# Kernel tuning notes

Hardware: AMD Instinct MI355X
Metric: run time of the kernel (lower is better)

The kernel has to match this reference:

```python
import jax, jax.numpy as jnp
import numpy as np

B, M, D, W = 4, 4096, 64, 128  # batch/heads, seq (m=n), head dim (k), nnz per row


def setup_inputs() -> dict:
    key = jax.random.key(0)
    kq, kk, kv, kc = jax.random.split(key, 4)
    q = jax.random.normal(kq, (B, M, D), dtype=jnp.float32)
    k = jax.random.normal(kk, (B, M, D), dtype=jnp.float32)
    v = jax.random.normal(kv, (B, M, D), dtype=jnp.float32)
    # CSR with uniform W nonzeros per row: row_offsets = arange(M+1)*W implicit,
    # column_indices flattened is [M*W]; stored here as [M, W].
    column_indices = jax.random.randint(kc, (M, W), 0, M).astype(jnp.int32)
    return {"q": q, "k": k, "v": v, "column_indices": column_indices}


def reference(q, k, v, column_indices):
    # SDDMM: logits[b,i,w] = <q[b,i,:], k[b, col[i,w], :]> at sparse positions only
    k_g = k[:, column_indices, :]                      # [B, M, W, D]
    logits = jnp.einsum('bmd,bmwd->bmw', q, k_g)       # sparse values per row
    # Sparse row-wise softmax (each CSR row has exactly W entries)
    weights = jax.nn.softmax(logits, axis=-1)          # [B, M, W]
    # SpMM: out[b,i,d] = sum_w weights[b,i,w] * v[b, col[i,w], d]
    v_g = v[:, column_indices, :]                      # [B, M, W, D]
    out = jnp.einsum('bmw,bmwd->bmd', weights, v_g)    # [B, M, D]
    return out
```

## Files before the change

kernel.cpp:

```cpp
#include <hip/hip_runtime.h>
#include <hip/hip_fp16.h>
#include <math.h>

constexpr int B = 4;
constexpr int M = 4096;
constexpr int D = 64;
constexpr int W = 128;
constexpr int NELEM = B * M * D;

__global__ __launch_bounds__(256) void cvt_f32_f16_2(
    const float4* __restrict__ k, const float4* __restrict__ v,
    __half2* __restrict__ kh, __half2* __restrict__ vh, int n4) {
    int i = blockIdx.x * 256 + threadIdx.x;
    const float4* src;
    __half2* dst;
    if (i < n4) { src = k; dst = kh; }
    else        { src = v; dst = vh; i -= n4; if (i >= n4) return; }
    float4 f = src[i];
    dst[2 * i]     = __floats2half2_rn(f.x, f.y);
    dst[2 * i + 1] = __floats2half2_rn(f.z, f.w);
}

__global__ __launch_bounds__(256, 4) void sparse_attn_f16(
    const float* __restrict__ q,
    const __half* __restrict__ kh,
    const __half* __restrict__ vh,
    const int*   __restrict__ idx,
    float*       __restrict__ out)
{
    const int blk  = blockIdx.x;
    const int b    = blk & 3;
    const int mb   = (blk >> 2) * 4;
    const int t    = threadIdx.x;
    const int wave = t >> 6;
    const int lane = t & 63;
    const int ci   = lane & 7;
    const int r    = lane >> 3;
    const int m    = mb + wave;

    __shared__ int idx_s[4 * W];

    ((int2*)idx_s)[t] = ((const int2*)(idx + (size_t)mb * W))[t];

    const float* qrow = q + ((size_t)b * M + m) * D;
    const float4 qa = ((const float4*)qrow)[2 * ci];
    const float4 qb = ((const float4*)qrow)[2 * ci + 1];

    __syncthreads();

    int off[16];
    #pragma unroll
    for (int j = 0; j < 16; ++j) off[j] = idx_s[wave * W + j * 8 + r];

    const __half* kb = kh + (size_t)b * M * D;
    const __half* vb = vh + (size_t)b * M * D;

    float larr[16];
    #pragma unroll
    for (int batch = 0; batch < 2; ++batch) {
        float4 kreg[8];
        #pragma unroll
        for (int jj = 0; jj < 8; ++jj) {
            const int j = batch * 8 + jj;
            kreg[jj] = *(const float4*)(kb + (size_t)off[j] * D + ci * 8);
        }
        #pragma unroll
        for (int jj = 0; jj < 8; ++jj) {
            const __half2* h = (const __half2*)&kreg[jj];
            float2 f0 = __half22float2(h[0]);
            float2 f1 = __half22float2(h[1]);
            float2 f2 = __half22float2(h[2]);
            float2 f3 = __half22float2(h[3]);
            float part = f0.x * qa.x + f0.y * qa.y + f1.x * qa.z + f1.y * qa.w
                       + f2.x * qb.x + f2.y * qb.y + f3.x * qb.z + f3.y * qb.w;
            part += __shfl_xor(part, 1);
            part += __shfl_xor(part, 2);
            part += __shfl_xor(part, 4);
            larr[batch * 8 + jj] = part;
        }
    }

    float mx = larr[0];
    #pragma unroll
    for (int j = 1; j < 16; ++j) mx = fmaxf(mx, larr[j]);
    mx = fmaxf(mx, __shfl_xor(mx, 8));
    mx = fmaxf(mx, __shfl_xor(mx, 16));
    mx = fmaxf(mx, __shfl_xor(mx, 32));

    float sum = 0.f;
    #pragma unroll
    for (int j = 0; j < 16; ++j) { larr[j] = __expf(larr[j] - mx); sum += larr[j]; }
    sum += __shfl_xor(sum, 8);
    sum += __shfl_xor(sum, 16);
    sum += __shfl_xor(sum, 32);
    const float inv = 1.0f / sum;

    float acc[8] = {0, 0, 0, 0, 0, 0, 0, 0};
    #pragma unroll
    for (int batch = 0; batch < 2; ++batch) {
        float4 vreg[8];
        #pragma unroll
        for (int jj = 0; jj < 8; ++jj) {
            const int j = batch * 8 + jj;
            vreg[jj] = *(const float4*)(vb + (size_t)off[j] * D + ci * 8);
        }
        #pragma unroll
        for (int jj = 0; jj < 8; ++jj) {
            const float p = larr[batch * 8 + jj];
            const __half2* h = (const __half2*)&vreg[jj];
            #pragma unroll
            for (int c = 0; c < 4; ++c) {
                float2 f = __half22float2(h[c]);
                acc[2 * c]     += p * f.x;
                acc[2 * c + 1] += p * f.y;
            }
        }
    }
    #pragma unroll
    for (int o = 8; o < 64; o <<= 1) {
        #pragma unroll
        for (int i = 0; i < 8; ++i) acc[i] += __shfl_xor(acc[i], o);
    }

    if (r == 0) {
        float4* orow = (float4*)(out + ((size_t)b * M + m) * D);
        orow[2 * ci]     = make_float4(acc[0] * inv, acc[1] * inv,
                                       acc[2] * inv, acc[3] * inv);
        orow[2 * ci + 1] = make_float4(acc[4] * inv, acc[5] * inv,
                                       acc[6] * inv, acc[7] * inv);
    }
}

__global__ __launch_bounds__(128) void sparse_attn_f32(
    const float* __restrict__ q,
    const float* __restrict__ k,
    const float* __restrict__ v,
    const int*   __restrict__ idx,
    float*       __restrict__ out)
{
    const int blk = blockIdx.x;
    const int b = blk & 3;
    const int m = blk >> 2;
    const int t = threadIdx.x;
    const int lane = t & 63;
    const int wave = t >> 6;
    const int ci = lane & 15;
    const int r  = lane >> 4;

    __shared__ int   idx_s[W];
    __shared__ float sc_s[W];
    __shared__ float red_s[4];
    __shared__ float4 opart_s[16];

    idx_s[t] = idx[m * W + t];
    const float4 qf = ((const float4*)(q + ((size_t)b * M + m) * D))[ci];
    __syncthreads();

    const float* kb = k + (size_t)b * M * D;
    const int wbase = wave * 64;

    #pragma unroll
    for (int j = 0; j < 16; ++j) {
        const int w = wbase + j * 4 + r;
        const float4 kv = ((const float4*)(kb + (size_t)idx_s[w] * D))[ci];
        float part = kv.x * qf.x + kv.y * qf.y + kv.z * qf.z + kv.w * qf.w;
        part += __shfl_xor(part, 1);
        part += __shfl_xor(part, 2);
        part += __shfl_xor(part, 4);
        part += __shfl_xor(part, 8);
        if (ci == 0) sc_s[w] = part;
    }
    __syncthreads();

    float logit = sc_s[t];
    float mx = logit;
    #pragma unroll
    for (int o = 1; o < 64; o <<= 1) mx = fmaxf(mx, __shfl_xor(mx, o));
    if (lane == 0) red_s[wave] = mx;
    __syncthreads();
    mx = fmaxf(red_s[0], red_s[1]);
    float e = __expf(logit - mx);
    float sm = e;
    #pragma unroll
    for (int o = 1; o < 64; o <<= 1) sm += __shfl_xor(sm, o);
    if (lane == 0) red_s[2 + wave] = sm;
    __syncthreads();
    const float inv_denom = 1.0f / (red_s[2] + red_s[3]);
    sc_s[t] = e * inv_denom;
    __syncthreads();

    const float* vb = v + (size_t)b * M * D;
    float4 acc = {0.f, 0.f, 0.f, 0.f};
    #pragma unroll
    for (int j = 0; j < 16; ++j) {
        const int w = wbase + j * 4 + r;
        const float p = sc_s[w];
        const float4 vv = ((const float4*)(vb + (size_t)idx_s[w] * D))[ci];
        acc.x += p * vv.x; acc.y += p * vv.y;
        acc.z += p * vv.z; acc.w += p * vv.w;
    }
    acc.x += __shfl_xor(acc.x, 16); acc.y += __shfl_xor(acc.y, 16);
    acc.z += __shfl_xor(acc.z, 16); acc.w += __shfl_xor(acc.w, 16);
    acc.x += __shfl_xor(acc.x, 32); acc.y += __shfl_xor(acc.y, 32);
    acc.z += __shfl_xor(acc.z, 32); acc.w += __shfl_xor(acc.w, 32);

    if (wave == 0 && r == 0) opart_s[ci] = acc;
    __syncthreads();
    if (wave == 1 && r == 0) {
        const float4 o0 = opart_s[ci];
        float4 res;
        res.x = o0.x + acc.x; res.y = o0.y + acc.y;
        res.z = o0.z + acc.z; res.w = o0.w + acc.w;
        ((float4*)(out + ((size_t)b * M + m) * D))[ci] = res;
    }
}

extern "C" void kernel_launch(void* const* d_in, const int* in_sizes, int n_in,
                              void* d_out, int out_size, void* d_ws, size_t ws_size,
                              hipStream_t stream) {
    const float* q = (const float*)d_in[0];
    const float* k = (const float*)d_in[1];
    const float* v = (const float*)d_in[2];
    const int* idx = (const int*)d_in[3];
    float* out = (float*)d_out;

    const size_t need = (size_t)2 * NELEM * sizeof(__half);
    if (ws_size >= need) {
        __half* kh = (__half*)d_ws;
        __half* vh = kh + NELEM;
        const int n4 = NELEM / 4;
        const int cblk = (2 * n4 + 255) / 256;
        cvt_f32_f16_2<<<cblk, 256, 0, stream>>>((const float4*)k, (const float4*)v,
                                                (__half2*)kh, (__half2*)vh, n4);
        sparse_attn_f16<<<B * M / 4, 256, 0, stream>>>(q, kh, vh, idx, out);
    } else {
        sparse_attn_f32<<<B * M, 128, 0, stream>>>(q, k, v, idx, out);
    }
}
```

Before: 95.99 us.

## Use fdot2 for QK, nontemporal gathers, and prefetch V before softmax

Converts q to fp16 and computes QK partial dot products with packed fdot2 instead of unpacking each half to float. K and V rows are gathered with nontemporal 128-bit loads using precomputed 32-bit byte offsets. The first batch of V rows is issued before the softmax reduction and the second right after it, so gather latency overlaps the softmax math. Rounding q to fp16 reduces dot-product precision, and the extra in-flight V registers may raise register pressure.

```diff
diff --git a/kernel.cpp b/kernel.cpp
--- a/kernel.cpp
+++ b/kernel.cpp
@@ -7,6 +7,9 @@
 constexpr int D = 64;
 constexpr int W = 128;
 constexpr int NELEM = B * M * D;
+
+typedef _Float16 h2_t __attribute__((ext_vector_type(2)));
+typedef int      i4_t __attribute__((ext_vector_type(4)));
 
 __global__ __launch_bounds__(256) void cvt_f32_f16_2(
     const float4* __restrict__ k, const float4* __restrict__ v,
@@ -45,34 +48,39 @@
     const float* qrow = q + ((size_t)b * M + m) * D;
     const float4 qa = ((const float4*)qrow)[2 * ci];
     const float4 qb = ((const float4*)qrow)[2 * ci + 1];
-
-    __syncthreads();
-
-    int off[16];
-    #pragma unroll
-    for (int j = 0; j < 16; ++j) off[j] = idx_s[wave * W + j * 8 + r];
-
-    const __half* kb = kh + (size_t)b * M * D;
-    const __half* vb = vh + (size_t)b * M * D;
+    h2_t qh[4];
+    qh[0] = (h2_t){(_Float16)qa.x, (_Float16)qa.y};
+    qh[1] = (h2_t){(_Float16)qa.z, (_Float16)qa.w};
+    qh[2] = (h2_t){(_Float16)qb.x, (_Float16)qb.y};
+    qh[3] = (h2_t){(_Float16)qb.z, (_Float16)qb.w};
+
+    __syncthreads();
+
+    int voff[16];
+    #pragma unroll
+    for (int j = 0; j < 16; ++j)
+        voff[j] = idx_s[wave * W + j * 8 + r] * (D * 2) + ci * 16;
+
+    const char* kb = (const char*)(kh + (size_t)b * M * D);
+    const char* vb = (const char*)(vh + (size_t)b * M * D);
 
     float larr[16];
     #pragma unroll
     for (int batch = 0; batch < 2; ++batch) {
-        float4 kreg[8];
+        i4_t kreg[8];
+        #pragma unroll
+        for (int jj = 0; jj < 8; ++jj)
+            kreg[jj] = __builtin_nontemporal_load(
+                (const i4_t*)(kb + voff[batch * 8 + jj]));
         #pragma unroll
         for (int jj = 0; jj < 8; ++jj) {
-            const int j = batch * 8 + jj;
-            kreg[jj] = *(const float4*)(kb + (size_t)off[j] * D + ci * 8);
-        }
-        #pragma unroll
-        for (int jj = 0; jj < 8; ++jj) {
-            const __half2* h = (const __half2*)&kreg[jj];
-            float2 f0 = __half22float2(h[0]);
-            float2 f1 = __half22float2(h[1]);
-            float2 f2 = __half22float2(h[2]);
-            float2 f3 = __half22float2(h[3]);
-            float part = f0.x * qa.x + f0.y * qa.y + f1.x * qa.z + f1.y * qa.w
-                       + f2.x * qb.x + f2.y * qb.y + f3.x * qb.z + f3.y * qb.w;
+            union { i4_t v; h2_t h[4]; } u;
+            u.v = kreg[jj];
+            float part = 0.f;
+            part = __builtin_amdgcn_fdot2(u.h[0], qh[0], part, false);
+            part = __builtin_amdgcn_fdot2(u.h[1], qh[1], part, false);
+            part = __builtin_amdgcn_fdot2(u.h[2], qh[2], part, false);
+            part = __builtin_amdgcn_fdot2(u.h[3], qh[3], part, false);
             part += __shfl_xor(part, 1);
             part += __shfl_xor(part, 2);
             part += __shfl_xor(part, 4);
@@ -80,6 +88,11 @@
         }
     }
 
+    i4_t vreg0[8];
+    #pragma unroll
+    for (int jj = 0; jj < 8; ++jj)
+        vreg0[jj] = __builtin_nontemporal_load((const i4_t*)(vb + voff[jj]));
+
     float mx = larr[0];
     #pragma unroll
     for (int j = 1; j < 16; ++j) mx = fmaxf(mx, larr[j]);
@@ -96,24 +109,31 @@
     const float inv = 1.0f / sum;
 
     float acc[8] = {0, 0, 0, 0, 0, 0, 0, 0};
-    #pragma unroll
-    for (int batch = 0; batch < 2; ++batch) {
-        float4 vreg[8];
-        #pragma unroll
-        for (int jj = 0; jj < 8; ++jj) {
-            const int j = batch * 8 + jj;
-            vreg[jj] = *(const float4*)(vb + (size_t)off[j] * D + ci * 8);
+    i4_t vreg1[8];
+    #pragma unroll
+    for (int jj = 0; jj < 8; ++jj)
+        vreg1[jj] = __builtin_nontemporal_load((const i4_t*)(vb + voff[8 + jj]));
+
+    #pragma unroll
+    for (int jj = 0; jj < 8; ++jj) {
+        const float p = larr[jj];
+        union { i4_t v; h2_t h[4]; } u;
+        u.v = vreg0[jj];
+        #pragma unroll
+        for (int c = 0; c < 4; ++c) {
+            acc[2 * c]     += p * (float)u.h[c][0];
+            acc[2 * c + 1] += p * (float)u.h[c][1];
         }
-        #pragma unroll
-        for (int jj = 0; jj < 8; ++jj) {
-            const float p = larr[batch * 8 + jj];
-            const __half2* h = (const __half2*)&vreg[jj];
-            #pragma unroll
-            for (int c = 0; c < 4; ++c) {
-                float2 f = __half22float2(h[c]);
-                acc[2 * c]     += p * f.x;
-                acc[2 * c + 1] += p * f.y;
-            }
+    }
+    #pragma unroll
+    for (int jj = 0; jj < 8; ++jj) {
+        const float p = larr[8 + jj];
+        union { i4_t v; h2_t h[4]; } u;
+        u.v = vreg1[jj];
+        #pragma unroll
+        for (int c = 0; c < 4; ++c) {
+            acc[2 * c]     += p * (float)u.h[c][0];
+            acc[2 * c + 1] += p * (float)u.h[c][1];
         }
     }
     #pragma unroll
```

New measurement: 93.72 us. 1.02x faster.
